# Kernel tuning notes

Hardware: AMD Instinct MI355X
Metric: run time of the kernel (lower is better)

The kernel has to match this reference:

```python
import jax, jax.numpy as jnp
import numpy as np

B = 128; D = 192; DI = 384; DS = 16; DR = 12; L = 17; DEPTH = 12
NH = 8; HD = D // NH; NCLS = 10; EPS = 1e-5


def setup_inputs() -> dict:
    key = jax.random.key(0)
    ks = iter(jax.random.split(key, 128))
    def rn(shape, s=0.02):
        return jax.random.normal(next(ks), shape, dtype=jnp.float32) * s
    inp = {"x": jax.random.normal(next(ks), (B, 8, 224, 16), dtype=jnp.float32)}
    inp["t_patch_w"] = rn((D, 8, 14, 16)); inp["t_patch_b"] = jnp.zeros((D,), jnp.float32)
    inp["f_patch_w"] = rn((D, 8, 224, 1)); inp["f_patch_b"] = jnp.zeros((D,), jnp.float32)
    inp["t_tok"] = rn((1, 1, D)); inp["f_tok"] = rn((1, 1, D))
    inp["t_pos"] = rn((1, L, D)); inp["f_pos"] = rn((1, L, D))
    for p in ("t", "f"):
        inp[p + "_norm_w"] = jnp.ones((DEPTH, D), jnp.float32)
        inp[p + "_in_proj"] = rn((DEPTH, 2 * DI, D))
        inp[p + "_conv_w"] = rn((DEPTH, DI, 4), 0.3)
        inp[p + "_conv_b"] = jnp.zeros((DEPTH, DI), jnp.float32)
        inp[p + "_x_proj"] = rn((DEPTH, DR + 2 * DS, DI))
        inp[p + "_dt_w"] = rn((DEPTH, DI, DR))
        inp[p + "_dt_b"] = rn((DEPTH, DI), 0.5)
        A = jnp.tile(jnp.arange(1, DS + 1, dtype=jnp.float32)[None, None, :], (DEPTH, DI, 1))
        inp[p + "_A_log"] = jnp.log(A)
        inp[p + "_D"] = jnp.ones((DEPTH, DI), jnp.float32)
        inp[p + "_out_proj"] = rn((DEPTH, D, DI))
    inp["att_t_w"] = rn((4, D, D)); inp["att_t_b"] = jnp.zeros((4, D), jnp.float32)
    inp["att_tf_w"] = rn((4, D, D)); inp["att_tf_b"] = jnp.zeros((4, D), jnp.float32)
    inp["cls1_w"] = rn((512, D)); inp["cls1_b"] = jnp.zeros((512,), jnp.float32)
    inp["cls2_w"] = rn((NCLS, 512)); inp["cls2_b"] = jnp.zeros((NCLS,), jnp.float32)
    inp["pos1_w"] = rn((512, D)); inp["pos1_b"] = jnp.zeros((512,), jnp.float32)
    inp["pos2_w"] = rn((3, 512)); inp["pos2_b"] = jnp.zeros((3,), jnp.float32)
    return inp


def silu(x):
    return x * jax.nn.sigmoid(x)


def patch_embed(x, w, b, stride):
    # Conv2d VALID, then flatten(2).transpose(1,2) -> (B, num_patch, D)
    y = jax.lax.conv_general_dilated(x, w, window_strides=stride, padding="VALID",
                                     dimension_numbers=("NCHW", "OIHW", "NCHW"))
    y = y + b[None, :, None, None]
    Bb, C, H, W = y.shape
    return y.reshape(Bb, C, H * W).transpose(0, 2, 1)


def rmsnorm(x, w):
    return x * jax.lax.rsqrt(jnp.mean(x * x, -1, keepdims=True) + EPS) * w


def mamba_mixer(x, in_proj, conv_w, conv_b, x_proj, dt_w, dt_b, A_log, Dp, out_proj):
    Bb, Ll, _ = x.shape
    xz = x @ in_proj.T                         # (B,L,2*DI)
    xx, z = xz[..., :DI], xz[..., DI:]
    # depthwise causal conv, kernel 4, left pad 3
    xp = jnp.pad(xx, ((0, 0), (3, 0), (0, 0)))
    xx = sum(xp[:, k:k + Ll, :] * conv_w[:, k] for k in range(4)) + conv_b
    xx = silu(xx)                              # (B,L,DI)
    dbl = xx @ x_proj.T                        # (B,L,DR+2*DS)
    dt = jax.nn.softplus(dbl[..., :DR] @ dt_w.T + dt_b)     # (B,L,DI)
    Bm = dbl[..., DR:DR + DS]                  # (B,L,DS)
    Cm = dbl[..., DR + DS:]                    # (B,L,DS)
    A = -jnp.exp(A_log)                        # (DI,DS)
    dA = jnp.exp(dt[..., None] * A)            # (B,L,DI,DS)
    dBx = dt[..., None] * Bm[:, :, None, :] * xx[..., None]

    def step(h, inputs):
        dA_l, dBx_l, C_l = inputs
        h = dA_l * h + dBx_l
        y = jnp.einsum("bcn,bn->bc", h, C_l)
        return h, y

    h0 = jnp.zeros((Bb, DI, DS), x.dtype)
    _, ys = jax.lax.scan(step, h0, (dA.transpose(1, 0, 2, 3),
                                    dBx.transpose(1, 0, 2, 3),
                                    Cm.transpose(1, 0, 2)))
    y = ys.transpose(1, 0, 2) + Dp * xx
    y = y * silu(z)
    return y @ out_proj.T


def backbone(x, norm_w, in_proj, conv_w, conv_b, x_proj, dt_w, dt_b, A_log, Dp, out_proj):
    residual = None
    for i in range(DEPTH):
        residual = x if residual is None else residual + x
        h = rmsnorm(residual, norm_w[i])
        x = mamba_mixer(h, in_proj[i], conv_w[i], conv_b[i], x_proj[i],
                        dt_w[i], dt_b[i], A_log[i], Dp[i], out_proj[i])
    return x


def cross_attn(q, kv, w, b):
    Bb, Lq, _ = q.shape; Lk = kv.shape[1]
    qh = (q @ w[0].T + b[0]).reshape(Bb, Lq, NH, HD).transpose(0, 2, 1, 3)
    kh = (kv @ w[1].T + b[1]).reshape(Bb, Lk, NH, HD).transpose(0, 2, 1, 3)
    vh = (kv @ w[2].T + b[2]).reshape(Bb, Lk, NH, HD).transpose(0, 2, 1, 3)
    att = jax.nn.softmax(jnp.einsum("bhqd,bhkd->bhqk", qh, kh) / np.float32(np.sqrt(HD)), axis=-1)
    o = jnp.einsum("bhqk,bhkd->bhqd", att, vh).transpose(0, 2, 1, 3).reshape(Bb, Lq, D)
    return o @ w[3].T + b[3]


def reference(x, t_patch_w, t_patch_b, f_patch_w, f_patch_b, t_tok, f_tok, t_pos, f_pos,
              t_norm_w, t_in_proj, t_conv_w, t_conv_b, t_x_proj, t_dt_w, t_dt_b, t_A_log, t_D, t_out_proj,
              f_norm_w, f_in_proj, f_conv_w, f_conv_b, f_x_proj, f_dt_w, f_dt_b, f_A_log, f_D, f_out_proj,
              att_t_w, att_t_b, att_tf_w, att_tf_b,
              cls1_w, cls1_b, cls2_w, cls2_b, pos1_w, pos1_b, pos2_w, pos2_b):
    Bb = x.shape[0]
    t = patch_embed(x, t_patch_w, t_patch_b, (14, 1))     # (B,16,D)
    f = patch_embed(x, f_patch_w, f_patch_b, (1, 1))      # (B,16,D)
    t = jnp.concatenate([t, jnp.broadcast_to(t_tok, (Bb, 1, D))], axis=1)
    f = jnp.concatenate([f, jnp.broadcast_to(f_tok, (Bb, 1, D))], axis=1)
    t = t + t_pos
    f = f + f_pos
    t = backbone(t, t_norm_w, t_in_proj, t_conv_w, t_conv_b, t_x_proj,
                 t_dt_w, t_dt_b, t_A_log, t_D, t_out_proj)
    f = backbone(f, f_norm_w, f_in_proj, f_conv_w, f_conv_b, f_x_proj,
                 f_dt_w, f_dt_b, f_A_log, f_D, f_out_proj)
    t1 = cross_attn(t, f, att_t_w, att_t_b)
    fusion = cross_attn(t1, f, att_tf_w, att_tf_b)
    fusion = t + fusion
    feat = fusion[:, -1, :]
    cls = jax.nn.relu(feat @ cls1_w.T + cls1_b) @ cls2_w.T + cls2_b
    pos = jax.nn.relu(feat @ pos1_w.T + pos1_b) @ pos2_w.T + pos2_b
    return (cls, pos)
```

## Files before the change

kernel.cpp:

```cpp
#include <hip/hip_runtime.h>
#include <math.h>

#define NB 128
#define SEQ 17
#define DM 192
#define DI 384
#define DEPTH 12
#define ROW (SEQ*DM)
#define NROWS 4352
#define N192 (NROWS*DM)
#define C1IP (DEPTH*2*DI*DM)
#define C2OP (DEPTH*DM*DI)
#define KEMB 1792
#define CEMB_STRIDE 786432

typedef __attribute__((ext_vector_type(8))) short bf16x8;
typedef __attribute__((ext_vector_type(4))) float f32x4;

struct MambaW {
  const float* norm_w;
  const float* in_proj;
  const float* conv_w;
  const float* conv_b;
  const float* x_proj;
  const float* dt_w;
  const float* dt_b;
  const float* A_log;
  const float* D;
  const float* out_proj;
};

__device__ __forceinline__ float dot4(float4 a, float4 b) {
  return a.x*b.x + a.y*b.y + a.z*b.z + a.w*b.w;
}
__device__ __forceinline__ unsigned short f2bf(float f) {
  unsigned int u = __float_as_uint(f);
  u += 0x7FFFu + ((u >> 16) & 1u);
  return (unsigned short)(u >> 16);
}
__device__ __forceinline__ float bf2f(unsigned short h) {
  return __uint_as_float(((unsigned int)h) << 16);
}
__device__ __forceinline__ void split2(float v, unsigned short& h, unsigned short& l) {
  h = f2bf(v);
  l = f2bf(v - bf2f(h));
}

__global__ __launch_bounds__(256) void decomp_kernel(
    const float* __restrict__ s0, const float* __restrict__ s1,
    unsigned short* __restrict__ hi, unsigned short* __restrict__ lo, int nquads)
{
  const float* s = blockIdx.y ? s1 : s0;
  size_t base = (size_t)blockIdx.y * nquads;
  for (size_t i = (size_t)blockIdx.x*256 + threadIdx.x; i < (size_t)nquads;
       i += (size_t)gridDim.x*256) {
    float4 v = ((const float4*)s)[i];
    ushort4 h, l;
    split2(v.x, h.x, l.x); split2(v.y, h.y, l.y);
    split2(v.z, h.z, l.z); split2(v.w, h.w, l.w);
    ((ushort4*)hi)[base + i] = h;
    ((ushort4*)lo)[base + i] = l;
  }
}

__global__ __launch_bounds__(256) void prep_kernel(
    const float* __restrict__ x, float* __restrict__ Af)
{
  const int t = threadIdx.x;
  const int b = blockIdx.x >> 3, c = blockIdx.x & 7;
  const float* xp = x + (size_t)(b*8 + c)*3584;
  __shared__ float ts[16][225];
  for (int idx = t; idx < 3584; idx += 256)
    ts[idx & 15][idx >> 4] = xp[idx];
  __syncthreads();
  for (int i4 = t; i4 < 896; i4 += 256) {
    const int p = i4 / 56, r4 = (i4 - p*56)*4;
    float4 v;
    v.x = ts[p][r4]; v.y = ts[p][r4+1]; v.z = ts[p][r4+2]; v.w = ts[p][r4+3];
    *(float4*)&Af[(size_t)(b*16 + p)*KEMB + c*224 + r4] = v;
  }
}

__global__ __launch_bounds__(256) void gemm_embed(
    const float* __restrict__ x, const float* __restrict__ Af,
    const float* __restrict__ Wt, const float* __restrict__ Wf,
    float* __restrict__ C)
{
  const int t = threadIdx.x;
  const int bidx = blockIdx.x;
  const int xcd = bidx & 7;
  const int s_  = bidx >> 3;
  const int mt  = s_ % 3;
  const int u   = s_ / 3;
  const int trio = xcd*32 + u;
  const int nt  = trio & 63;
  const int kz  = trio >> 6;

  __shared__ float As[32][68];
  __shared__ float Bs[32][68];

  const float* Wsel = (nt < 32 ? Wt : Wf) + (size_t)(mt*64)*KEMB;

  const int srow = t >> 2;
  const int a8   = t & 3;
  const int sw   = (a8 & 1) << 4;
  const int colA = srow ^ sw;

  const int tn = t & 15;
  const int tm = t >> 4;
  float acc[4][4];
#pragma unroll
  for (int i = 0; i < 4; ++i)
#pragma unroll
    for (int j = 0; j < 4; ++j) acc[i][j] = 0.f;

  const int kbase = kz*448;
  const float* xrowbase = nullptr;
  const float* afrow    = nullptr;
  if (nt < 32) {
    const int r = nt*64 + srow;
    const int b = r >> 4, p = r & 15;
    xrowbase = x + (size_t)(b*8)*3584 + p*224 + a8*8;
  } else {
    const int r = (nt - 32)*64 + srow;
    afrow = Af + (size_t)r*KEMB + kbase + a8*8;
  }
  const float* brow = Wsel + (size_t)srow*KEMB + kbase + a8*8;

  int cblk = kz*2, rr = 0;
  float4 pa0, pa1, pb0, pb1;
  {
    const float* ar = (nt < 32) ? (xrowbase + (size_t)cblk*3584 + rr) : afrow;
    pa0 = *(const float4*)(ar + 0);
    pa1 = *(const float4*)(ar + 4);
    pb0 = *(const float4*)(brow + 0);
    pb1 = *(const float4*)(brow + 4);
  }

  for (int kt = 0; kt < 448; kt += 32) {
    As[a8*8+0][colA]=pa0.x; As[a8*8+1][colA]=pa0.y;
    As[a8*8+2][colA]=pa0.z; As[a8*8+3][colA]=pa0.w;
    As[a8*8+4][colA]=pa1.x; As[a8*8+5][colA]=pa1.y;
    As[a8*8+6][colA]=pa1.z; As[a8*8+7][colA]=pa1.w;
    Bs[a8*8+0][colA]=pb0.x; Bs[a8*8+1][colA]=pb0.y;
    Bs[a8*8+2][colA]=pb0.z; Bs[a8*8+3][colA]=pb0.w;
    Bs[a8*8+4][colA]=pb1.x; Bs[a8*8+5][colA]=pb1.y;
    Bs[a8*8+6][colA]=pb1.z; Bs[a8*8+7][colA]=pb1.w;
    __syncthreads();
    if (kt + 32 < 448) {
      rr += 32; if (rr == 224) { rr = 0; ++cblk; }
      const float* ar = (nt < 32) ? (xrowbase + (size_t)cblk*3584 + rr)
                                  : (afrow + kt + 32);
      pa0 = *(const float4*)(ar + 0);
      pa1 = *(const float4*)(ar + 4);
      const float* br = brow + kt + 32;
      pb0 = *(const float4*)(br + 0);
      pb1 = *(const float4*)(br + 4);
    }
#pragma unroll
    for (int kk = 0; kk < 32; ++kk) {
      const int xr = ((kk >> 3) & 1) << 4;
      float a[4], b[4];
      *(float4*)&a[0] = *(const float4*)&As[kk][(tn*4) ^ xr];
      *(float4*)&b[0] = *(const float4*)&Bs[kk][(tm*4) ^ xr];
#pragma unroll
      for (int i = 0; i < 4; ++i)
#pragma unroll
        for (int j = 0; j < 4; ++j) acc[i][j] = fmaf(a[i], b[j], acc[i][j]);
    }
    __syncthreads();
  }

  float* Cb = C + (size_t)kz*CEMB_STRIDE
            + (size_t)(nt*64 + tn*4)*DM + mt*64 + tm*4;
#pragma unroll
  for (int i = 0; i < 4; ++i)
    *(float4*)(Cb + (size_t)i*DM) = *(float4*)&acc[i][0];
}

template<int MT>
__global__ __launch_bounds__(256) void gemm_mfma(
    const unsigned short* __restrict__ Ahi, const unsigned short* __restrict__ Alo, int lda,
    const unsigned short* __restrict__ BtHi, const unsigned short* __restrict__ BtLo,
    const unsigned short* __restrict__ BfHi, const unsigned short* __restrict__ BfLo,
    int ldb, int kchunk, float* __restrict__ C, int ldc, long ckstride)
{
  const int t = threadIdx.x;
  const int mt = blockIdx.x, nt = blockIdx.y, kz = blockIdx.z;
  __shared__ alignas(16) unsigned short sAh[64*40], sAl[64*40];
  __shared__ alignas(16) unsigned short sBh[MT*40], sBl[MT*40];

  const bool isT = (nt < 34);
  const unsigned short* aH = Ahi + (size_t)(nt*64)*lda + kz*kchunk;
  const unsigned short* aL = Alo + (size_t)(nt*64)*lda + kz*kchunk;
  const unsigned short* bH = (isT ? BtHi : BfHi) + (size_t)(mt*MT)*ldb + kz*kchunk;
  const unsigned short* bL = (isT ? BtLo : BfLo) + (size_t)(mt*MT)*ldb + kz*kchunk;

  const int wave = t >> 6, lane = t & 63;
  const int arow = wave*16 + (lane & 15);
  const int kb   = (lane >> 4) * 8;

  f32x4 acc[MT/16];
#pragma unroll
  for (int mb = 0; mb < MT/16; ++mb) acc[mb] = (f32x4){0.f, 0.f, 0.f, 0.f};

  const int srow = t >> 2, sseg = (t & 3) * 8;

  for (int kt = 0; kt < kchunk; kt += 32) {
    __syncthreads();
    *(uint4*)(sAh + srow*40 + sseg) = *(const uint4*)(aH + (size_t)srow*lda + kt + sseg);
    *(uint4*)(sAl + srow*40 + sseg) = *(const uint4*)(aL + (size_t)srow*lda + kt + sseg);
#pragma unroll
    for (int rep = 0; rep < MT/64; ++rep) {
      int r2 = rep*64 + srow;
      *(uint4*)(sBh + r2*40 + sseg) = *(const uint4*)(bH + (size_t)r2*ldb + kt + sseg);
      *(uint4*)(sBl + r2*40 + sseg) = *(const uint4*)(bL + (size_t)r2*ldb + kt + sseg);
    }
    __syncthreads();
    bf16x8 ah = *(const bf16x8*)(sAh + arow*40 + kb);
    bf16x8 al = *(const bf16x8*)(sAl + arow*40 + kb);
#pragma unroll
    for (int mb = 0; mb < MT/16; ++mb) {
      bf16x8 bh = *(const bf16x8*)(sBh + (mb*16 + (lane & 15))*40 + kb);
      bf16x8 bl = *(const bf16x8*)(sBl + (mb*16 + (lane & 15))*40 + kb);
      acc[mb] = __builtin_amdgcn_mfma_f32_16x16x32_bf16(al, bh, acc[mb], 0, 0, 0);
      acc[mb] = __builtin_amdgcn_mfma_f32_16x16x32_bf16(ah, bl, acc[mb], 0, 0, 0);
      acc[mb] = __builtin_amdgcn_mfma_f32_16x16x32_bf16(ah, bh, acc[mb], 0, 0, 0);
    }
  }

  float* Cb = C + (long)kz*ckstride
            + (size_t)(nt*64 + wave*16 + (lane >> 4)*4)*ldc + mt*MT + (lane & 15);
#pragma unroll
  for (int mb = 0; mb < MT/16; ++mb)
#pragma unroll
    for (int r = 0; r < 4; ++r)
      Cb[(size_t)r*ldc + mb*16] = acc[mb][r];
}

__global__ __launch_bounds__(192) void embed_fin_kernel(
    const float* __restrict__ Cg,
    const float* __restrict__ bT, const float* __restrict__ posT,
    const float* __restrict__ tokT, const float* __restrict__ nwT,
    const float* __restrict__ bF, const float* __restrict__ posF,
    const float* __restrict__ tokF, const float* __restrict__ nwF,
    float* __restrict__ res,
    unsigned short* __restrict__ hHi, unsigned short* __restrict__ hLo)
{
  const int d = threadIdx.x;
  const int sb = blockIdx.x;
  const int is_f = sb >> 7, b = sb & 127;
  const float* bias = is_f ? bF : bT;
  const float* pos  = is_f ? posF : posT;
  const float* tok  = is_f ? tokF : tokT;
  const float* nw   = is_f ? nwF : nwT;
  __shared__ float sq[SEQ*192];
  __shared__ float pt[SEQ*8];
  __shared__ float sc[SEQ];

  float v[SEQ];
  const float* Crow = Cg + ((size_t)is_f*2048 + (size_t)b*16)*DM + d;
  const float add = bias[d];
#pragma unroll
  for (int l = 0; l < 16; ++l) {
    v[l] = (Crow[l*DM] + Crow[(size_t)CEMB_STRIDE + l*DM])
         + (Crow[(size_t)2*CEMB_STRIDE + l*DM] + Crow[(size_t)3*CEMB_STRIDE + l*DM])
         + add + pos[l*DM + d];
    sq[l*192 + d] = v[l]*v[l];
  }
  v[16] = tok[d] + pos[16*DM + d];
  sq[16*192 + d] = v[16]*v[16];
  __syncthreads();
  if (d < 136) {
    int l = d >> 3, j = d & 7;
    float s = 0.f;
#pragma unroll
    for (int q = 0; q < 24; ++q) s += sq[l*192 + j + 8*q];
    pt[d] = s;
  }
  __syncthreads();
  if (d < SEQ) {
    float s = 0.f;
#pragma unroll
    for (int j = 0; j < 8; ++j) s += pt[d*8 + j];
    sc[d] = rsqrtf(s*(1.0f/192.0f) + 1e-5f);
  }
  __syncthreads();
  float nwd = nw[d];
#pragma unroll
  for (int l = 0; l < SEQ; ++l) {
    size_t idx = ((size_t)sb*SEQ + l)*DM + d;
    res[idx] = v[l];
    unsigned short h, lo_;
    split2(v[l]*sc[l]*nwd, h, lo_);
    hHi[idx] = h; hLo[idx] = lo_;
  }
}

__global__ __launch_bounds__(384) void mid_kernel(
    const float* __restrict__ xzg,
    unsigned short* __restrict__ yHi, unsigned short* __restrict__ yLo,
    MambaW wt, MambaW wf, int layer)
{
  const int t = threadIdx.x;
  const int sb = blockIdx.x;
  const MambaW W = (sb >= NB) ? wf : wt;
  __shared__ alignas(16) float lds_xx[SEQ*388];
  __shared__ alignas(16) float lds_dbl[748];
  const size_t nb = (size_t)sb*SEQ;

  float xr[SEQ];
  {
    const float4 cw = ((const float4*)(W.conv_w + (size_t)layer*DI*4))[t];
    const float cb = W.conv_b[layer*DI + t];
    float p0 = 0.f, p1 = 0.f, p2 = 0.f;
#pragma unroll
    for (int l = 0; l < SEQ; ++l) {
      float xz = xzg[(nb + l)*768 + t];
      float v = cb + xz*cw.w + p0*cw.z + p1*cw.y + p2*cw.x;
      p2 = p1; p1 = p0; p0 = xz;
      v = v / (1.f + __expf(-v));
      xr[l] = v;
      lds_xx[l*388 + t] = v;
    }
  }
  __syncthreads();

  {
    const float* XP = W.x_proj + (size_t)layer*44*DI;
#pragma unroll
    for (int rep = 0; rep < 2; ++rep) {
      int o = t + rep*384;
      if (o < 748) {
        int j = o / 17, l = o - j*17;
        const float4* wr = (const float4*)(XP + j*DI);
        const float4* xv4 = (const float4*)lds_xx + l*97;
        float a = 0.f;
        for (int k4 = 0; k4 < 96; ++k4) a += dot4(xv4[k4], wr[k4]);
        lds_dbl[l*44 + j] = a;
      }
    }
  }
  __syncthreads();

  {
    const int c = t;
    const float* dwr = W.dt_w + (size_t)layer*DI*12 + c*12;
    float w0[12];
#pragma unroll
    for (int r = 0; r < 12; ++r) w0[r] = dwr[r];
    const float dtb = W.dt_b[layer*DI + c];
    const float4* alr = (const float4*)(W.A_log + (size_t)layer*DI*16) + c*4;
    float Av[16];
#pragma unroll
    for (int q = 0; q < 4; ++q) {
      float4 a4 = alr[q];
      Av[q*4+0] = -__expf(a4.x); Av[q*4+1] = -__expf(a4.y);
      Av[q*4+2] = -__expf(a4.z); Av[q*4+3] = -__expf(a4.w);
    }
    const float Dp = W.D[layer*DI + c];
    float hst[16];
#pragma unroll
    for (int n = 0; n < 16; ++n) hst[n] = 0.f;
    for (int l = 0; l < SEQ; ++l) {
      float a = dtb;
#pragma unroll
      for (int r = 0; r < 12; ++r) a += lds_dbl[l*44 + r]*w0[r];
      float dt = (a > 20.f) ? a : log1pf(__expf(a));
      float xv = xr[l];
      const float4* dbv = (const float4*)(lds_dbl + l*44 + 12);
      float4 Bq[4], Cq[4];
      Bq[0]=dbv[0]; Bq[1]=dbv[1]; Bq[2]=dbv[2]; Bq[3]=dbv[3];
      Cq[0]=dbv[4]; Cq[1]=dbv[5]; Cq[2]=dbv[6]; Cq[3]=dbv[7];
      const float* Bs = (const float*)Bq;
      const float* Cs = (const float*)Cq;
      float y = 0.f;
      float dbx = dt * xv;
#pragma unroll
      for (int n = 0; n < 16; ++n) {
        float dA = __expf(dt * Av[n]);
        float hn = dA*hst[n] + dbx*Bs[n];
        hst[n] = hn;
        y += hn*Cs[n];
      }
      y += Dp * xv;
      float zv = xzg[(nb + l)*768 + DI + c];
      y *= zv / (1.f + __expf(-zv));
      unsigned short h, lo_;
      split2(y, h, lo_);
      size_t idx = (nb + l)*DI + c;
      yHi[idx] = h; yLo[idx] = lo_;
    }
  }
}

__global__ __launch_bounds__(192) void fuse_kernel(
    const float* __restrict__ part, float* __restrict__ res,
    unsigned short* __restrict__ hHi, unsigned short* __restrict__ hLo,
    float* __restrict__ xfin,
    const float* __restrict__ nwT, const float* __restrict__ nwF,
    int layer, int last)
{
  const int d = threadIdx.x;
  const int sb = blockIdx.x;
  const size_t nb = (size_t)sb*SEQ;
  __shared__ float sq[SEQ*192];
  __shared__ float pt[SEQ*8];
  __shared__ float sc[SEQ];

  float v[SEQ];
#pragma unroll
  for (int l = 0; l < SEQ; ++l) {
    size_t idx = (nb + l)*DM + d;
    float s = part[idx] + part[(size_t)N192 + idx];
    if (!last) {
      s += res[idx];
      res[idx] = s;
      v[l] = s;
      sq[l*192 + d] = s*s;
    } else {
      xfin[idx] = s;
    }
  }
  if (last) return;
  __syncthreads();
  if (d < 136) {
    int l = d >> 3, j = d & 7;
    float s = 0.f;
#pragma unroll
    for (int q = 0; q < 24; ++q) s += sq[l*192 + j + 8*q];
    pt[d] = s;
  }
  __syncthreads();
  if (d < SEQ) {
    float s = 0.f;
#pragma unroll
    for (int j = 0; j < 8; ++j) s += pt[d*8 + j];
    sc[d] = rsqrtf(s*(1.0f/192.0f) + 1e-5f);
  }
  __syncthreads();
  const float* nw = ((sb < NB) ? nwT : nwF) + (size_t)(layer + 1)*DM;
  float nwd = nw[d];
#pragma unroll
  for (int l = 0; l < SEQ; ++l) {
    unsigned short h, lo_;
    split2(v[l]*sc[l]*nwd, h, lo_);
    size_t idx = (nb + l)*DM + d;
    hHi[idx] = h; hLo[idx] = lo_;
  }
}

__global__ __launch_bounds__(256, 3) void gemm_kv(
    const float* __restrict__ A, int lda, int ktot,
    const float* __restrict__ Bt, const float* __restrict__ Bf, int ldb,
    const float* __restrict__ bias1, const float* __restrict__ bias2,
    float* __restrict__ C, int ldc)
{
  const int t  = threadIdx.x;
  const int mt = blockIdx.x, nt = blockIdx.y;
  __shared__ float As[32][132];
  __shared__ float Bs[32][100];

  int pass = mt >> 2, kv = (mt >> 1) & 1, half = mt & 1;
  const float* Bp = (pass ? Bf : Bt) + (size_t)(1+kv)*DM*DM + (size_t)(half*96)*ldb;
  const float* bp = (pass ? bias2 : bias1) + (1+kv)*DM + half*96;
  const float* Ap = A + (size_t)(nt*128)*lda;

  const int tn = t & 15, tm = t >> 4;
  float acc[8][6];
#pragma unroll
  for (int i = 0; i < 8; ++i)
#pragma unroll
    for (int j = 0; j < 6; ++j) acc[i][j] = 0.f;

  const int srow = t >> 1;
  const int skl  = (t & 1) * 16;

  for (int kt = 0; kt < ktot; kt += 32) {
    __syncthreads();
    {
      const float* ar = Ap + (size_t)srow*lda + kt + skl;
      float4 v0 = *(const float4*)(ar + 0);
      float4 v1 = *(const float4*)(ar + 4);
      float4 v2 = *(const float4*)(ar + 8);
      float4 v3 = *(const float4*)(ar + 12);
      As[skl+ 0][srow]=v0.x; As[skl+ 1][srow]=v0.y; As[skl+ 2][srow]=v0.z; As[skl+ 3][srow]=v0.w;
      As[skl+ 4][srow]=v1.x; As[skl+ 5][srow]=v1.y; As[skl+ 6][srow]=v1.z; As[skl+ 7][srow]=v1.w;
      As[skl+ 8][srow]=v2.x; As[skl+ 9][srow]=v2.y; As[skl+10][srow]=v2.z; As[skl+11][srow]=v2.w;
      As[skl+12][srow]=v3.x; As[skl+13][srow]=v3.y; As[skl+14][srow]=v3.z; As[skl+15][srow]=v3.w;
    }
    if (srow < 96) {
      const float* br = Bp + (size_t)srow*ldb + kt + skl;
      float4 v0 = *(const float4*)(br + 0);
      float4 v1 = *(const float4*)(br + 4);
      float4 v2 = *(const float4*)(br + 8);
      float4 v3 = *(const float4*)(br + 12);
      Bs[skl+ 0][srow]=v0.x; Bs[skl+ 1][srow]=v0.y; Bs[skl+ 2][srow]=v0.z; Bs[skl+ 3][srow]=v0.w;
      Bs[skl+ 4][srow]=v1.x; Bs[skl+ 5][srow]=v1.y; Bs[skl+ 6][srow]=v1.z; Bs[skl+ 7][srow]=v1.w;
      Bs[skl+ 8][srow]=v2.x; Bs[skl+ 9][srow]=v2.y; Bs[skl+10][srow]=v2.z; Bs[skl+11][srow]=v2.w;
      Bs[skl+12][srow]=v3.x; Bs[skl+13][srow]=v3.y; Bs[skl+14][srow]=v3.z; Bs[skl+15][srow]=v3.w;
    }
    __syncthreads();
#pragma unroll
    for (int kk = 0; kk < 32; ++kk) {
      float a[8], b[6];
      *(float4*)&a[0] = *(const float4*)&As[kk][tn*4];
      *(float4*)&a[4] = *(const float4*)&As[kk][64 + tn*4];
      *(float2*)&b[0] = *(const float2*)&Bs[kk][tm*6];
      *(float2*)&b[2] = *(const float2*)&Bs[kk][tm*6+2];
      *(float2*)&b[4] = *(const float2*)&Bs[kk][tm*6+4];
#pragma unroll
      for (int i = 0; i < 8; ++i)
#pragma unroll
        for (int j = 0; j < 6; ++j) acc[i][j] = fmaf(a[i], b[j], acc[i][j]);
    }
  }

  float* Cb = C + (size_t)(nt*128)*ldc + mt*96;
#pragma unroll
  for (int ni = 0; ni < 8; ++ni) {
    int n = (ni < 4) ? tn*4 + ni : 64 + tn*4 + (ni - 4);
    float* cr = Cb + (size_t)n*ldc;
#pragma unroll
    for (int j = 0; j < 6; ++j) cr[tm*6 + j] = acc[ni][j] + bp[tm*6 + j];
  }
}

__device__ __forceinline__ void coop_gemv192(
    const float* __restrict__ W, const float* __restrict__ bias,
    const float* __restrict__ xv, float* __restrict__ y,
    const float* __restrict__ addv, int nout, int relu,
    float* __restrict__ wbuf, float* __restrict__ pt, int t)
{
  float pv[48];
#pragma unroll
  for (int i = 0; i < 48; ++i) pv[i] = W[t + i*256];
  for (int d0 = 0; d0 < nout; d0 += 64) {
    {
      int r0 = t / 192;
      int c0 = t - r0*192;
      int addr = r0*193 + c0;
      int c = c0;
#pragma unroll
      for (int i = 0; i < 48; ++i) {
        wbuf[addr] = pv[i];
        c += 64;
        const int wrap = (c >= 192);
        c -= wrap ? 192 : 0;
        addr += wrap ? 258 : 257;
      }
    }
    __syncthreads();
    if (d0 + 64 < nout) {
      const float* nsrc = W + (size_t)(d0+64)*192;
#pragma unroll
      for (int i = 0; i < 48; ++i) pv[i] = nsrc[t + i*256];
    }
    {
      const int ol = t & 63, ks = t >> 6;
      const float* wr = wbuf + ol*193 + ks*48;
      const float* xr = xv + ks*48;
      float a = 0.f;
#pragma unroll
      for (int k = 0; k < 48; ++k) a = fmaf(wr[k], xr[k], a);
      pt[ks*64 + ol] = a;
    }
    __syncthreads();
    if (t < 64) {
      float s = (pt[t] + pt[64+t]) + (pt[128+t] + pt[192+t]) + bias[d0+t];
      if (addv) s += addv[d0+t];
      if (relu) s = fmaxf(s, 0.f);
      y[d0+t] = s;
    }
    __syncthreads();
  }
}

__global__ __launch_bounds__(256) void attn_core_kernel(
    const float* __restrict__ xfin, const float* __restrict__ kvg,
    const float* __restrict__ w1, const float* __restrict__ b1,
    const float* __restrict__ w2, const float* __restrict__ b2,
    const float* __restrict__ c1w, const float* __restrict__ c1b,
    const float* __restrict__ c2w, const float* __restrict__ c2b,
    const float* __restrict__ p1w, const float* __restrict__ p1b,
    const float* __restrict__ p2w, const float* __restrict__ p2b,
    float* __restrict__ out)
{
  const int t = threadIdx.x;
  const int b = blockIdx.x >> 1;
  const int path = blockIdx.x & 1;
  __shared__ float wbuf[64*193];
  __shared__ float pt[256];
  __shared__ float pth[256];
  __shared__ alignas(16) float t16[DM];
  __shared__ alignas(16) float qv[DM];
  __shared__ alignas(16) float ov[DM];
  __shared__ alignas(16) float t1[DM];
  __shared__ alignas(16) float feat[DM];
  __shared__ alignas(16) float hbuf[512];

  if (t < DM) t16[t] = xfin[((size_t)b*SEQ + 16)*DM + t];
  __syncthreads();

  for (int pass = 0; pass < 2; ++pass) {
    const float* wa = pass ? w2 : w1;
    const float* ba = pass ? b2 : b1;
    coop_gemv192(wa, ba, pass ? t1 : t16, qv, nullptr, DM, 0, wbuf, pt, t);
    if (t < DM) {
      int h = t / 24;
      float4 q0 = *(const float4*)&qv[h*24];
      float4 q1 = *(const float4*)&qv[h*24+4];
      float4 q2 = *(const float4*)&qv[h*24+8];
      float4 q3 = *(const float4*)&qv[h*24+12];
      float4 q4 = *(const float4*)&qv[h*24+16];
      float4 q5 = *(const float4*)&qv[h*24+20];
      float scs[SEQ];
      float mx = -1e30f;
#pragma unroll
      for (int lk = 0; lk < SEQ; ++lk) {
        const float4* kr = (const float4*)(kvg + ((size_t)b*SEQ + lk)*768 + pass*384 + h*24);
        float s_ = dot4(q0,kr[0]) + dot4(q1,kr[1]) + dot4(q2,kr[2])
                 + dot4(q3,kr[3]) + dot4(q4,kr[4]) + dot4(q5,kr[5]);
        s_ *= 0.20412414523193154f;
        scs[lk] = s_;
        mx = fmaxf(mx, s_);
      }
      float den = 0.f;
#pragma unroll
      for (int lk = 0; lk < SEQ; ++lk) { float e = __expf(scs[lk]-mx); scs[lk]=e; den += e; }
      float inv = 1.f/den;
      float o = 0.f;
#pragma unroll
      for (int lk = 0; lk < SEQ; ++lk)
        o += scs[lk] * kvg[((size_t)b*SEQ + lk)*768 + pass*384 + DM + t];
      ov[t] = o*inv;
    }
    __syncthreads();
    coop_gemv192(wa + 3*DM*DM, ba + 3*DM, ov, pass ? feat : t1,
                 pass ? t16 : nullptr, DM, 0, wbuf, pt, t);
  }

  coop_gemv192(path ? p1w : c1w, path ? p1b : c1b, feat, hbuf,
               nullptr, 512, 1, wbuf, pt, t);

  {
    const int op = t & 15, ks = t >> 4;
    const int nop = path ? 3 : 10;
    float a = 0.f;
    if (op < nop) {
      const float* wr = (path ? p2w : c2w) + (size_t)op*512 + ks*32;
      const float4* w4 = (const float4*)wr;
      const float4* v4 = (const float4*)(hbuf + ks*32);
#pragma unroll
      for (int j = 0; j < 8; ++j) a += dot4(v4[j], w4[j]);
    }
    pth[op*16 + ks] = a;
  }
  __syncthreads();
  if (t < (path ? 3 : 10)) {
    float s = 0.f;
#pragma unroll
    for (int j = 0; j < 16; ++j) s += pth[t*16 + j];
    if (!path) out[b*10 + t] = s + c2b[t];
    else       out[1280 + b*3 + t] = s + p2b[t];
  }
}

extern "C" void kernel_launch(void* const* d_in, const int* in_sizes, int n_in,
                              void* d_out, int out_size, void* d_ws, size_t ws_size,
                              hipStream_t stream)
{
  (void)in_sizes; (void)n_in; (void)out_size; (void)ws_size;
  const float* x    = (const float*)d_in[0];
  const float* tpw  = (const float*)d_in[1];
  const float* tpb  = (const float*)d_in[2];
  const float* fpw  = (const float*)d_in[3];
  const float* fpb  = (const float*)d_in[4];
  const float* ttok = (const float*)d_in[5];
  const float* ftok = (const float*)d_in[6];
  const float* tpos = (const float*)d_in[7];
  const float* fpos = (const float*)d_in[8];
  MambaW wt { (const float*)d_in[9],  (const float*)d_in[10], (const float*)d_in[11],
              (const float*)d_in[12], (const float*)d_in[13], (const float*)d_in[14],
              (const float*)d_in[15], (const float*)d_in[16], (const float*)d_in[17],
              (const float*)d_in[18] };
  MambaW wf { (const float*)d_in[19], (const float*)d_in[20], (const float*)d_in[21],
              (const float*)d_in[22], (const float*)d_in[23], (const float*)d_in[24],
              (const float*)d_in[25], (const float*)d_in[26], (const float*)d_in[27],
              (const float*)d_in[28] };
  const float* attw  = (const float*)d_in[29];
  const float* attb  = (const float*)d_in[30];
  const float* attw2 = (const float*)d_in[31];
  const float* attb2 = (const float*)d_in[32];
  const float* c1w = (const float*)d_in[33];
  const float* c1b = (const float*)d_in[34];
  const float* c2w = (const float*)d_in[35];
  const float* c2b = (const float*)d_in[36];
  const float* p1w = (const float*)d_in[37];
  const float* p1b = (const float*)d_in[38];
  const float* p2w = (const float*)d_in[39];
  const float* p2b = (const float*)d_in[40];

  float* ws = (float*)d_ws;
  size_t off = 0;
  float* res  = ws + off; off += (size_t)N192;
  float* xfin = ws + off; off += (size_t)N192;
  float* xzg  = ws + off; off += (size_t)4*N192;
  float* part = ws + off; off += (size_t)2*N192;
  unsigned short* hHi = (unsigned short*)(ws + off); off += (size_t)N192/2;
  unsigned short* hLo = (unsigned short*)(ws + off); off += (size_t)N192/2;
  unsigned short* yHi = (unsigned short*)(ws + off); off += (size_t)N192;
  unsigned short* yLo = (unsigned short*)(ws + off); off += (size_t)N192;
  unsigned short* ipHi = (unsigned short*)(ws + off); off += (size_t)C1IP;
  unsigned short* ipLo = (unsigned short*)(ws + off); off += (size_t)C1IP;
  unsigned short* opHi = (unsigned short*)(ws + off); off += (size_t)C2OP;
  unsigned short* opLo = (unsigned short*)(ws + off); off += (size_t)C2OP;
  float* kvg = part;

  float* Cemb = ws + (size_t)N192;
  float* Af   = ws + (size_t)N192 + (size_t)4*CEMB_STRIDE;

  decomp_kernel<<<dim3(512, 2), 256, 0, stream>>>(wt.in_proj, wf.in_proj,
                                                  ipHi, ipLo, C1IP/4);
  decomp_kernel<<<dim3(512, 2), 256, 0, stream>>>(wt.out_proj, wf.out_proj,
                                                  opHi, opLo, C2OP/4);
  prep_kernel<<<1024, 256, 0, stream>>>(x, Af);
  gemm_embed<<<768, 256, 0, stream>>>(x, Af, tpw, fpw, Cemb);
  embed_fin_kernel<<<256, 192, 0, stream>>>(Cemb,
      tpb, tpos, ttok, wt.norm_w,
      fpb, fpos, ftok, wf.norm_w,
      res, hHi, hLo);

  for (int i = 0; i < DEPTH; ++i) {
    const size_t ipo = (size_t)i*2*DI*DM;
    const size_t opo = (size_t)i*DM*DI;
    gemm_mfma<64><<<dim3(12, 68, 1), 256, 0, stream>>>(
        hHi, hLo, DM,
        ipHi + ipo, ipLo + ipo, ipHi + C1IP + ipo, ipLo + C1IP + ipo,
        DM, DM , xzg, 768, 0);
    mid_kernel<<<256, 384, 0, stream>>>(xzg, yHi, yLo, wt, wf, i);
    gemm_mfma<64><<<dim3(3, 68, 2), 256, 0, stream>>>(
        yHi, yLo, DI,
        opHi + opo, opLo + opo, opHi + C2OP + opo, opLo + C2OP + opo,
        DI, 192, part, DM, (long)N192);
    fuse_kernel<<<256, 192, 0, stream>>>(part, res, hHi, hLo, xfin,
        wt.norm_w, wf.norm_w, i, (i == DEPTH-1) ? 1 : 0);
  }

  gemm_kv<<<dim3(8, 17), 256, 0, stream>>>(
      xfin + (size_t)NB*ROW, DM, DM,
      attw, attw2, DM, attb, attb2, kvg, 768);
  attn_core_kernel<<<256, 256, 0, stream>>>(xfin, kvg,
      attw, attb, attw2, attb2,
      c1w, c1b, c2w, c2b, p1w, p1b, p2w, p2b, (float*)d_out);
}
```

Measured before the change: 1.137 ms.

## Split fuse kernel per token, vectorize gemv LDS staging, prefetch gate values

The residual-add/RMSNorm fuse kernel now launches one block per token row (256x17 grid) instead of one block per sequence, which gives far more parallelism and uses less shared memory per block. The cooperative gemv in the attention kernel now stages weights through LDS as float2 with a 97-float2 row pitch. The mid kernel preloads all gate z values into registers before the scan and unrolls the x_proj dot loop. These trade more blocks and barriers, plus extra register pressure in the scan, for better latency hiding and wider memory accesses.

After: 1.034 ms. -9.1%, faster.

```diff
diff --git a/kernel.cpp b/kernel.cpp
--- a/kernel.cpp
+++ b/kernel.cpp
@@ -336,6 +336,7 @@
         const float4* wr = (const float4*)(XP + j*DI);
         const float4* xv4 = (const float4*)lds_xx + l*97;
         float a = 0.f;
+#pragma unroll 8
         for (int k4 = 0; k4 < 96; ++k4) a += dot4(xv4[k4], wr[k4]);
         lds_dbl[l*44 + j] = a;
       }
@@ -359,6 +360,10 @@
       Av[q*4+2] = -__expf(a4.z); Av[q*4+3] = -__expf(a4.w);
     }
     const float Dp = W.D[layer*DI + c];
+    float zr[SEQ];
+#pragma unroll
+    for (int l = 0; l < SEQ; ++l)
+      zr[l] = xzg[(nb + l)*768 + DI + c];
     float hst[16];
 #pragma unroll
     for (int n = 0; n < 16; ++n) hst[n] = 0.f;
@@ -384,7 +389,7 @@
         y += hn*Cs[n];
       }
       y += Dp * xv;
-      float zv = xzg[(nb + l)*768 + DI + c];
+      float zv = zr[l];
       y *= zv / (1.f + __expf(-zv));
       unsigned short h, lo_;
       split2(y, h, lo_);
@@ -402,52 +407,36 @@
     int layer, int last)
 {
   const int d = threadIdx.x;
-  const int sb = blockIdx.x;
-  const size_t nb = (size_t)sb*SEQ;
-  __shared__ float sq[SEQ*192];
-  __shared__ float pt[SEQ*8];
-  __shared__ float sc[SEQ];
-
-  float v[SEQ];
-#pragma unroll
-  for (int l = 0; l < SEQ; ++l) {
-    size_t idx = (nb + l)*DM + d;
-    float s = part[idx] + part[(size_t)N192 + idx];
-    if (!last) {
-      s += res[idx];
-      res[idx] = s;
-      v[l] = s;
-      sq[l*192 + d] = s*s;
-    } else {
-      xfin[idx] = s;
-    }
-  }
-  if (last) return;
-  __syncthreads();
-  if (d < 136) {
-    int l = d >> 3, j = d & 7;
-    float s = 0.f;
-#pragma unroll
-    for (int q = 0; q < 24; ++q) s += sq[l*192 + j + 8*q];
-    pt[d] = s;
-  }
-  __syncthreads();
-  if (d < SEQ) {
-    float s = 0.f;
-#pragma unroll
-    for (int j = 0; j < 8; ++j) s += pt[d*8 + j];
-    sc[d] = rsqrtf(s*(1.0f/192.0f) + 1e-5f);
+  const int sb = blockIdx.x, l = blockIdx.y;
+  const size_t idx = ((size_t)sb*SEQ + l)*DM + d;
+  __shared__ float sq[192];
+  __shared__ float pt[8];
+  __shared__ float sc;
+
+  float s = part[idx] + part[(size_t)N192 + idx];
+  if (last) { xfin[idx] = s; return; }
+  s += res[idx];
+  res[idx] = s;
+  sq[d] = s*s;
+  __syncthreads();
+  if (d < 8) {
+    float p = 0.f;
+#pragma unroll
+    for (int q = 0; q < 24; ++q) p += sq[d + 8*q];
+    pt[d] = p;
+  }
+  __syncthreads();
+  if (d == 0) {
+    float ssum = 0.f;
+#pragma unroll
+    for (int j = 0; j < 8; ++j) ssum += pt[j];
+    sc = rsqrtf(ssum*(1.0f/192.0f) + 1e-5f);
   }
   __syncthreads();
   const float* nw = ((sb < NB) ? nwT : nwF) + (size_t)(layer + 1)*DM;
-  float nwd = nw[d];
-#pragma unroll
-  for (int l = 0; l < SEQ; ++l) {
-    unsigned short h, lo_;
-    split2(v[l]*sc[l]*nwd, h, lo_);
-    size_t idx = (nb + l)*DM + d;
-    hHi[idx] = h; hLo[idx] = lo_;
-  }
+  unsigned short h, lo_;
+  split2(s*sc*nw[d], h, lo_);
+  hHi[idx] = h; hLo[idx] = lo_;
 }
 
 __global__ __launch_bounds__(256, 3) void gemm_kv(
@@ -532,37 +521,38 @@
     const float* __restrict__ addv, int nout, int relu,
     float* __restrict__ wbuf, float* __restrict__ pt, int t)
 {
-  float pv[48];
-#pragma unroll
-  for (int i = 0; i < 48; ++i) pv[i] = W[t + i*256];
+  float2 pv[24];
+  const float2* W2 = (const float2*)W;
+#pragma unroll
+  for (int i = 0; i < 24; ++i) pv[i] = W2[t + i*256];
   for (int d0 = 0; d0 < nout; d0 += 64) {
     {
-      int r0 = t / 192;
-      int c0 = t - r0*192;
-      int addr = r0*193 + c0;
-      int c = c0;
-#pragma unroll
-      for (int i = 0; i < 48; ++i) {
-        wbuf[addr] = pv[i];
-        c += 64;
-        const int wrap = (c >= 192);
-        c -= wrap ? 192 : 0;
-        addr += wrap ? 258 : 257;
+      float2* wb2 = (float2*)wbuf;
+#pragma unroll
+      for (int i = 0; i < 24; ++i) {
+        const int g = t + i*256;
+        const int r = g / 96;
+        const int c2 = g - r*96;
+        wb2[r*97 + c2] = pv[i];
       }
     }
     __syncthreads();
     if (d0 + 64 < nout) {
-      const float* nsrc = W + (size_t)(d0+64)*192;
-#pragma unroll
-      for (int i = 0; i < 48; ++i) pv[i] = nsrc[t + i*256];
+      const float2* nsrc = (const float2*)(W + (size_t)(d0+64)*192);
+#pragma unroll
+      for (int i = 0; i < 24; ++i) pv[i] = nsrc[t + i*256];
     }
     {
       const int ol = t & 63, ks = t >> 6;
-      const float* wr = wbuf + ol*193 + ks*48;
-      const float* xr = xv + ks*48;
+      const float2* wr2 = (const float2*)wbuf + ol*97 + ks*24;
+      const float2* xr2 = (const float2*)(xv + ks*48);
       float a = 0.f;
 #pragma unroll
-      for (int k = 0; k < 48; ++k) a = fmaf(wr[k], xr[k], a);
+      for (int k = 0; k < 24; ++k) {
+        float2 w2 = wr2[k], x2 = xr2[k];
+        a = fmaf(w2.x, x2.x, a);
+        a = fmaf(w2.y, x2.y, a);
+      }
       pt[ks*64 + ol] = a;
     }
     __syncthreads();
@@ -589,7 +579,7 @@
   const int t = threadIdx.x;
   const int b = blockIdx.x >> 1;
   const int path = blockIdx.x & 1;
-  __shared__ float wbuf[64*193];
+  __shared__ alignas(16) float wbuf[64*194];
   __shared__ float pt[256];
   __shared__ float pth[256];
   __shared__ alignas(16) float t16[DM];
@@ -743,7 +733,7 @@
         yHi, yLo, DI,
         opHi + opo, opLo + opo, opHi + C2OP + opo, opLo + C2OP + opo,
         DI, 192, part, DM, (long)N192);
-    fuse_kernel<<<256, 192, 0, stream>>>(part, res, hHi, hLo, xfin,
+    fuse_kernel<<<dim3(256, 17), 192, 0, stream>>>(part, res, hHi, hLo, xfin,
         wt.norm_w, wf.norm_w, i, (i == DEPTH-1) ? 1 : 0);
   }
 
```
